# Kernel optimization log

Measured on AMD Instinct MI355X. Metric: run time of the kernel, lower is better.

The kernel has to match this reference:

```python
import jax, jax.numpy as jnp
import numpy as np

N, M, D_IN, H1, D, OUT_C = 2048, 128, 352, 512, 256, 13


def _lin_bn_relu(x, w, b, g, be):
    # 1x1 conv == linear over last dim; BN (eval) folded to per-channel affine (g, be)
    return jax.nn.relu(g * (x @ w.T + b) + be)


def _encode(x, wA, bA, gA, beA, wB, bB, gB, beB):
    return _lin_bn_relu(_lin_bn_relu(x, wA, bA, gA, beA), wB, bB, gB, beB)


def setup_inputs() -> dict:
    key = jax.random.key(0)
    ks = iter(jax.random.split(key, 64))

    def wgt(shape, s=0.05):
        return (jax.random.normal(next(ks), shape, jnp.float32) * s)

    def gamma(c):
        return 1.0 + 0.05 * jax.random.normal(next(ks), (c,), jnp.float32)

    inp = {}
    inp['ext_fea'] = jax.random.normal(next(ks), (N, D_IN), jnp.float32)
    inp['lab_fea'] = jax.random.normal(next(ks), (M, D_IN), jnp.float32)
    # convs1: 352->512->256, each Conv1d(1x1)+BN+ReLU
    inp.update(w1a=wgt((H1, D_IN)), b1a=wgt((H1,)), g1a=gamma(H1), be1a=wgt((H1,)))
    inp.update(w1b=wgt((D, H1)), b1b=wgt((D,)), g1b=gamma(D), be1b=wgt((D,)))
    # convs2: same shapes
    inp.update(w2a=wgt((H1, D_IN)), b2a=wgt((H1,)), g2a=gamma(H1), be2a=wgt((H1,)))
    inp.update(w2b=wgt((D, H1)), b2b=wgt((D,)), g2b=gamma(D), be2b=wgt((D,)))
    # wei_conv SharedMLP [256,32,64,256]: three Conv2d(1x1)+BN+ReLU
    inp.update(mw1=wgt((32, D)), mb1=wgt((32,)), mg1=gamma(32), mbe1=wgt((32,)))
    inp.update(mw2=wgt((64, 32)), mb2=wgt((64,)), mg2=gamma(64), mbe2=wgt((64,)))
    inp.update(mw3=wgt((D, 64)), mb3=wgt((D,)), mg3=gamma(D), mbe3=wgt((D,)))
    # fc
    inp.update(fcw=wgt((OUT_C, D)), fcb=wgt((OUT_C,)))
    return inp


def reference(ext_fea, lab_fea,
              w1a, b1a, g1a, be1a, w1b, b1b, g1b, be1b,
              w2a, b2a, g2a, be2a, w2b, b2b, g2b, be2b,
              mw1, mb1, mg1, mbe1, mw2, mb2, mg2, mbe2, mw3, mb3, mg3, mbe3,
              fcw, fcb):
    A = _encode(ext_fea, w1a, b1a, g1a, be1a, w1b, b1b, g1b, be1b)   # [N, 256]
    B = _encode(lab_fea, w2a, b2a, g2a, be2a, w2b, b2b, g2b, be2b)   # [M, 256]
    diff = A[:, None, :] - B[None, :, :]                             # [N, M, 256]
    h = _lin_bn_relu(diff, mw1, mb1, mg1, mbe1)                      # [N, M, 32]
    h = _lin_bn_relu(h, mw2, mb2, mg2, mbe2)                         # [N, M, 64]
    wei = _lin_bn_relu(h, mw3, mb3, mg3, mbe3)                       # [N, M, 256]
    # torch softmax over dim=-1 of [1,256,N,M] == over M == axis 1 here
    wei = jax.nn.softmax(wei, axis=1)
    att = jnp.sum(wei * diff, axis=1)                                # [N, 256]
    return att @ fcw.T + fcb                                         # [N, 13]
```

## Files before the change

### kernel.cpp

```cpp
#include <hip/hip_runtime.h>
#include <stdint.h>


typedef __attribute__((ext_vector_type(4))) float float4_t;
typedef __attribute__((ext_vector_type(4))) float f32x4;
typedef __attribute__((ext_vector_type(8))) short bf16x8;
typedef __attribute__((ext_vector_type(8))) unsigned short ushort8_t;
typedef unsigned short ushort_t;

__device__ __forceinline__ unsigned short f2b(float f) {
  union { float f; unsigned int i; } v; v.f = f;
  unsigned int x = v.i;
  return (unsigned short)((x + 0x7FFFu + ((x >> 16) & 1u)) >> 16);
}

template<int ISBF>
__device__ __forceinline__ ushort8_t ld8(const void* base, size_t idx) {
  if constexpr (ISBF) {
    return *(const ushort8_t*)((const ushort_t*)base + idx);
  } else {
    const float* p = (const float*)base + idx;
    float4_t v0 = *(const float4_t*)p;
    float4_t v1 = *(const float4_t*)(p + 4);
    ushort8_t u;
    #pragma unroll
    for (int e = 0; e < 4; ++e) { u[e] = f2b(v0[e]); u[4 + e] = f2b(v1[e]); }
    return u;
  }
}

template<int XBF, int WBF, int OUT_BF16>
__global__ __launch_bounds__(256) void enc_mfma(
    const void* __restrict__ XA, const void* __restrict__ WA,
    const float* __restrict__ bA, const float* __restrict__ gA, const float* __restrict__ beA,
    void* __restrict__ YA,
    const void* __restrict__ XB, const void* __restrict__ WB,
    const float* __restrict__ bB, const float* __restrict__ gB, const float* __restrict__ beB,
    void* __restrict__ YB, float* __restrict__ YBT,
    int J, int K, int nbxA)
{
  __shared__ ushort_t Xs[2][32][40];
  __shared__ ushort_t Ws[2][32][40];
  const int bx = blockIdx.x, by = blockIdx.y;
  const void* X; const void* W;
  const float *bb, *gg, *bev; void* Y; int i0, isB;
  if (bx < nbxA) { X = XA; W = WA; bb = bA; gg = gA; bev = beA; Y = YA; i0 = bx * 32; isB = 0; }
  else           { X = XB; W = WB; bb = bB; gg = gB; bev = beB; Y = YB; i0 = (bx - nbxA) * 32; isB = 1; }
  const int j0 = by * 32;
  const int tid = threadIdx.x, w = tid >> 6, lane = tid & 63, lg = lane >> 4, lr = lane & 15;
  const int mt = w >> 1, ct = w & 1;
  const int row = tid >> 2, k8 = (tid & 3) * 8;

  f32x4 acc = f32x4{0.f, 0.f, 0.f, 0.f};

  ushort8_t sv = (row < 32) ? ld8<XBF>(X, (size_t)(i0 + row) * K + k8)
                            : ld8<WBF>(W, (size_t)(j0 + row - 32) * K + k8);
  for (int kt = 0; kt < K; kt += 32) {
    const int buf = (kt >> 5) & 1;
    if (row < 32) *(ushort8_t*)&Xs[buf][row][k8] = sv;
    else          *(ushort8_t*)&Ws[buf][row - 32][k8] = sv;
    __syncthreads();
    if (kt + 32 < K)
      sv = (row < 32) ? ld8<XBF>(X, (size_t)(i0 + row) * K + kt + 32 + k8)
                      : ld8<WBF>(W, (size_t)(j0 + row - 32) * K + kt + 32 + k8);
    bf16x8 af = *(const bf16x8*)&Xs[buf][mt * 16 + lr][lg * 8];
    bf16x8 bf_ = *(const bf16x8*)&Ws[buf][ct * 16 + lr][lg * 8];
    acc = __builtin_amdgcn_mfma_f32_16x16x32_bf16(af, bf_, acc, 0, 0, 0);
  }
  const int c = j0 + ct * 16 + lr;
  const float g = gg[c], bv = bb[c], ev = bev[c];
  #pragma unroll
  for (int r = 0; r < 4; ++r) {
    const int rowo = i0 + mt * 16 + 4 * lg + r;
    float t = fmaxf(g * (acc[r] + bv) + ev, 0.f);
    if (OUT_BF16) ((ushort_t*)Y)[(size_t)rowo * J + c] = f2b(t);
    else {
      ((float*)Y)[(size_t)rowo * J + c] = t;
      if (isB && YBT) YBT[(size_t)c * 128 + rowo] = t;
    }
  }
}

__global__ __launch_bounds__(256) void proj32(
    const float* __restrict__ Aenc, const float* __restrict__ Benc,
    const float* __restrict__ mw1, const float* __restrict__ mb1,
    const float* __restrict__ mg1, const float* __restrict__ mbe1,
    float* __restrict__ PA2, float* __restrict__ PB2, int nbxA,
    const float* __restrict__ mw2, const float* __restrict__ mw3,
    ushort_t* __restrict__ mw2b, ushort_t* __restrict__ mw3b)
{
  __shared__ float ps[4][32];
  const int tid = threadIdx.x, bx = blockIdx.x;
  if (bx >= nbxA + 32) {
    const int g = (bx - nbxA - 32) * 256 + tid;
    const float* s; ushort_t* d; int j;
    if (g < 256) { s = mw2; d = mw2b; j = g; }
    else         { s = mw3; d = mw3b; j = g - 256; }
    float4_t v0 = *(const float4_t*)&s[(size_t)j * 8];
    float4_t v1 = *(const float4_t*)&s[(size_t)j * 8 + 4];
    ushort8_t u;
    #pragma unroll
    for (int e = 0; e < 4; ++e) { u[e] = f2b(v0[e]); u[4 + e] = f2b(v1[e]); }
    *(ushort8_t*)&d[(size_t)j * 8] = u;
    return;
  }
  const float* X; float* P; int n0, wb;
  if (bx < nbxA) { X = Aenc; P = PA2; n0 = bx * 4; wb = 1; }
  else           { X = Benc; P = PB2; n0 = (bx - nbxA) * 4; wb = 0; }
  const int k = tid & 31, r = (tid >> 5) & 3, half = tid >> 7;
  const int n = n0 + r;
  const float* xp = &X[(size_t)n * 256 + half * 128];
  const float* wp = &mw1[k * 256 + half * 128];
  float s = 0.f;
  #pragma unroll 8
  for (int q = 0; q < 128; q += 4) {
    float4_t xv = *(const float4_t*)&xp[q];
    float4_t wv = *(const float4_t*)&wp[q];
    #pragma unroll
    for (int e = 0; e < 4; ++e) s = fmaf(xv[e], wv[e], s);
  }
  if (half == 1) ps[r][k] = s;
  __syncthreads();
  if (half == 0) {
    s += ps[r][k];
    P[(size_t)n * 32 + k] = wb ? (mg1[k] * (s + mb1[k]) + mbe1[k]) : (mg1[k] * s);
  }
}

__global__ __launch_bounds__(256, 2) void main_attn(
    const float* __restrict__ PA2, const float* __restrict__ PB2,
    const float* __restrict__ A, const float* __restrict__ BmT,
    const ushort_t* __restrict__ mw2b, const float* __restrict__ mb2,
    const float* __restrict__ mg2, const float* __restrict__ mbe2,
    const ushort_t* __restrict__ mw3b, const float* __restrict__ mb3,
    const float* __restrict__ mg3, const float* __restrict__ mbe3,
    const float* __restrict__ fcw, const float* __restrict__ fcb,
    float* __restrict__ outp)
{
  __shared__ __align__(16) char smem[40576];
  float* attLs = (float*)(smem + 36864);
  float* part  = (float*)(smem + 38912);

  const int tid = threadIdx.x;
  const int w = tid >> 6, lane = tid & 63, lg = lane >> 4, lr = lane & 15;
  const int n0 = blockIdx.x * 2;
  const float LOG2E = 1.4426950408889634f;

  float g2h[4], b2h[4], e2h[4];
  #pragma unroll
  for (int jt = 0; jt < 4; ++jt) {
    const int j = jt * 16 + lr;
    g2h[jt] = mg2[j]; b2h[jt] = mb2[j]; e2h[jt] = mbe2[j];
  }
  float gs3[4], cs3[4];
  #pragma unroll
  for (int ct = 0; ct < 4; ++ct) {
    const int c = w * 64 + ct * 16 + lr;
    const float g = mg3[c];
    gs3[ct] = g * LOG2E;
    cs3[ct] = (g * mb3[c] + mbe3[c]) * LOG2E;
  }

  #pragma unroll
  for (int nn = 0; nn < 2; ++nn) {
    const int n = n0 + nn;
    ushort_t* h2s = (ushort_t*)(smem + nn * 18432);

    {
      f32x4 acc1[2][4];
      #pragma unroll
      for (int mt = 0; mt < 2; ++mt)
        #pragma unroll
        for (int jt = 0; jt < 4; ++jt) acc1[mt][jt] = f32x4{0.f, 0.f, 0.f, 0.f};
      bf16x8 a1[2], b1[4];
      {
        const float* pa = &PA2[(size_t)n * 32 + lg * 8];
        float4_t pa0 = *(const float4_t*)pa;
        float4_t pa1 = *(const float4_t*)(pa + 4);
        #pragma unroll
        for (int mt = 0; mt < 2; ++mt) {
          const int m = w * 32 + mt * 16 + lr;
          const float* pb = &PB2[(size_t)m * 32 + lg * 8];
          float4_t pb0 = *(const float4_t*)pb;
          float4_t pb1 = *(const float4_t*)(pb + 4);
          bf16x8 u;
          #pragma unroll
          for (int e = 0; e < 4; ++e) {
            u[e]     = (short)f2b(fmaxf(pa0[e] - pb0[e], 0.f));
            u[4 + e] = (short)f2b(fmaxf(pa1[e] - pb1[e], 0.f));
          }
          a1[mt] = u;
        }
      }
      #pragma unroll
      for (int jt = 0; jt < 4; ++jt)
        b1[jt] = *(const bf16x8*)&mw2b[(jt * 16 + lr) * 32 + lg * 8];
      #pragma unroll
      for (int mt = 0; mt < 2; ++mt)
        #pragma unroll
        for (int jt = 0; jt < 4; ++jt)
          acc1[mt][jt] = __builtin_amdgcn_mfma_f32_16x16x32_bf16(a1[mt], b1[jt], acc1[mt][jt], 0, 0, 0);
      #pragma unroll
      for (int jt = 0; jt < 4; ++jt) {
        #pragma unroll
        for (int mt = 0; mt < 2; ++mt)
          #pragma unroll
          for (int r = 0; r < 4; ++r)
            h2s[(w * 32 + mt * 16 + 4 * lg + r) * 72 + jt * 16 + lr] =
                f2b(fmaxf(g2h[jt] * (acc1[mt][jt][r] + b2h[jt]) + e2h[jt], 0.f));
      }
    }
    __syncthreads();

    float smv[4], wbv[4];
    #pragma unroll
    for (int cp = 0; cp < 2; ++cp) {
      f32x4 acc[8][2];
      #pragma unroll
      for (int mt = 0; mt < 8; ++mt) {
        acc[mt][0] = f32x4{0.f, 0.f, 0.f, 0.f};
        acc[mt][1] = f32x4{0.f, 0.f, 0.f, 0.f};
      }
      #pragma unroll
      for (int ks = 0; ks < 2; ++ks) {
        bf16x8 bfr[2];
        #pragma unroll
        for (int q = 0; q < 2; ++q) {
          const int c = w * 64 + (cp * 2 + q) * 16 + lr;
          bfr[q] = *(const bf16x8*)&mw3b[(size_t)c * 64 + ks * 32 + lg * 8];
        }
        #pragma unroll
        for (int mt = 0; mt < 8; ++mt) {
          bf16x8 af = *(const bf16x8*)&h2s[(mt * 16 + lr) * 72 + ks * 32 + lg * 8];
          acc[mt][0] = __builtin_amdgcn_mfma_f32_16x16x32_bf16(af, bfr[0], acc[mt][0], 0, 0, 0);
          acc[mt][1] = __builtin_amdgcn_mfma_f32_16x16x32_bf16(af, bfr[1], acc[mt][1], 0, 0, 0);
        }
      }
      #pragma unroll
      for (int q = 0; q < 2; ++q) {
        const int ct = cp * 2 + q;
        const int c = w * 64 + ct * 16 + lr;
        f32x4 sm4 = f32x4{0.f, 0.f, 0.f, 0.f};
        f32x4 wb4 = f32x4{0.f, 0.f, 0.f, 0.f};
        #pragma unroll
        for (int mt = 0; mt < 8; ++mt) {
          float4_t bv4 = *(const float4_t*)&BmT[(size_t)c * 128 + mt * 16 + 4 * lg];
          #pragma unroll
          for (int r = 0; r < 4; ++r) {
            float t = fmaf(gs3[ct], acc[mt][q][r], cs3[ct]);
            float p = exp2f(__builtin_amdgcn_fmed3f(t, 0.f, 80.f));
            sm4[r] += p;
            wb4[r] = fmaf(p, bv4[r], wb4[r]);
          }
        }
        smv[ct] = (sm4[0] + sm4[1]) + (sm4[2] + sm4[3]);
        wbv[ct] = (wb4[0] + wb4[1]) + (wb4[2] + wb4[3]);
      }
    }
    #pragma unroll
    for (int st = 16; st <= 32; st <<= 1) {
      #pragma unroll
      for (int ct = 0; ct < 4; ++ct) {
        smv[ct] += __shfl_xor(smv[ct], st, 64);
        wbv[ct] += __shfl_xor(wbv[ct], st, 64);
      }
    }
    if (lg == 0) {
      #pragma unroll
      for (int ct = 0; ct < 4; ++ct) {
        const int c = w * 64 + ct * 16 + lr;
        attLs[nn * 256 + c] = A[(size_t)n * 256 + c] - wbv[ct] / smv[ct];
      }
    }
  }
  __syncthreads();

  {
    const int o = tid >> 4, gp = tid & 15;
    if (o < 13) {
      float4_t wv[4];
      #pragma unroll
      for (int i = 0; i < 4; ++i)
        wv[i] = *(const float4_t*)&fcw[(size_t)o * 256 + gp * 16 + i * 4];
      #pragma unroll
      for (int nn = 0; nn < 2; ++nn) {
        float s = 0.f;
        #pragma unroll
        for (int i = 0; i < 4; ++i) {
          float4_t av = *(const float4_t*)&attLs[nn * 256 + gp * 16 + i * 4];
          #pragma unroll
          for (int e = 0; e < 4; ++e) s = fmaf(av[e], wv[i][e], s);
        }
        part[nn * 208 + o * 16 + gp] = s;
      }
    }
  }
  __syncthreads();
  if (tid < 26) {
    const int nn = tid / 13, o = tid % 13;
    float s = fcb[o];
    #pragma unroll
    for (int gp = 0; gp < 16; ++gp) s += part[nn * 208 + o * 16 + gp];
    outp[(size_t)(n0 + nn) * 13 + o] = s;
  }
}

extern "C" void kernel_launch(void* const* d_in, const int* in_sizes, int n_in,
                              void* d_out, int out_size, void* d_ws, size_t ws_size,
                              hipStream_t stream)
{
  const float* ext = (const float*)d_in[0];
  const float* lab = (const float*)d_in[1];
  const float* w1a = (const float*)d_in[2];
  const float* b1a = (const float*)d_in[3];
  const float* g1a = (const float*)d_in[4];
  const float* be1a= (const float*)d_in[5];
  const float* w1b = (const float*)d_in[6];
  const float* b1b = (const float*)d_in[7];
  const float* g1b = (const float*)d_in[8];
  const float* be1b= (const float*)d_in[9];
  const float* w2a = (const float*)d_in[10];
  const float* b2a = (const float*)d_in[11];
  const float* g2a = (const float*)d_in[12];
  const float* be2a= (const float*)d_in[13];
  const float* w2b = (const float*)d_in[14];
  const float* b2b = (const float*)d_in[15];
  const float* g2b = (const float*)d_in[16];
  const float* be2b= (const float*)d_in[17];
  const float* mw1 = (const float*)d_in[18];
  const float* mb1 = (const float*)d_in[19];
  const float* mg1 = (const float*)d_in[20];
  const float* mbe1= (const float*)d_in[21];
  const float* mw2 = (const float*)d_in[22];
  const float* mb2 = (const float*)d_in[23];
  const float* mg2 = (const float*)d_in[24];
  const float* mbe2= (const float*)d_in[25];
  const float* mw3 = (const float*)d_in[26];
  const float* mb3 = (const float*)d_in[27];
  const float* mg3 = (const float*)d_in[28];
  const float* mbe3= (const float*)d_in[29];
  const float* fcw = (const float*)d_in[30];
  const float* fcb = (const float*)d_in[31];

  char* ws = (char*)d_ws;
  ushort_t* Y1ab = (ushort_t*)(ws);
  float*    PA2  = (float*)(ws);
  float*    PB2  = (float*)(ws + 262144);
  float*    Aenc = (float*)(ws + (2u << 20));
  char* b5 = ws + (4u << 20);
  ushort_t* mw2b = (ushort_t*)(b5);
  ushort_t* mw3b = (ushort_t*)(b5 + 4096);
  ushort_t* Y1bb = (ushort_t*)(b5 + 36864);
  float*    Benc = (float*)(b5 + 167936);
  float*    BencT= (float*)(b5 + 299008);

  enc_mfma<0, 0, 1><<<dim3(68, 16), 256, 0, stream>>>(
      (const void*)ext, (const void*)w1a, b1a, g1a, be1a, (void*)Y1ab,
      (const void*)lab, (const void*)w2a, b2a, g2a, be2a, (void*)Y1bb,
      (float*)nullptr, 512, 352, 64);
  enc_mfma<1, 0, 0><<<dim3(68, 8), 256, 0, stream>>>(
      (const void*)Y1ab, (const void*)w1b, b1b, g1b, be1b, (void*)Aenc,
      (const void*)Y1bb, (const void*)w2b, b2b, g2b, be2b, (void*)Benc,
      BencT, 256, 512, 64);
  proj32<<<553, 256, 0, stream>>>(Aenc, Benc, mw1, mb1, mg1, mbe1, PA2, PB2, 512,
                                  mw2, mw3, mw2b, mw3b);
  main_attn<<<1024, 256, 0, stream>>>(PA2, PB2, Aenc, BencT,
                                      mw2b, mb2, mg2, mbe2, mw3b, mb3, mg3, mbe3,
                                      fcw, fcb, (float*)d_out);
}
```

Baseline: 87.79 us.

## Double main attention block to 512 threads, halving per-wave channel work

The main attention kernel now runs 8 waves per block instead of 4. Each wave handles 16 rows of the first MFMA stage and 32 output channels of the second, instead of 32 and 64, so the two-pass channel loop goes away and per-thread accumulators shrink. The final FC reduction is spread over 32 partial sums per output. exp2f is also replaced by the raw hardware exp2 intrinsic. The aim is more parallelism and latency hiding per CU, at the cost of more threads sharing the same LDS tile and barriers.

Result: slower. 95.07 us (+8.3%).

```diff
diff --git a/kernel.cpp b/kernel.cpp
--- a/kernel.cpp
+++ b/kernel.cpp
@@ -127,7 +127,7 @@
   }
 }
 
-__global__ __launch_bounds__(256, 2) void main_attn(
+__global__ __launch_bounds__(512, 2) void main_attn(
     const float* __restrict__ PA2, const float* __restrict__ PB2,
     const float* __restrict__ A, const float* __restrict__ BmT,
     const ushort_t* __restrict__ mw2b, const float* __restrict__ mb2,
@@ -137,7 +137,7 @@
     const float* __restrict__ fcw, const float* __restrict__ fcb,
     float* __restrict__ outp)
 {
-  __shared__ __align__(16) char smem[40576];
+  __shared__ __align__(16) char smem[42240];
   float* attLs = (float*)(smem + 36864);
   float* part  = (float*)(smem + 38912);
 
@@ -152,10 +152,10 @@
     const int j = jt * 16 + lr;
     g2h[jt] = mg2[j]; b2h[jt] = mb2[j]; e2h[jt] = mbe2[j];
   }
-  float gs3[4], cs3[4];
+  float gs3[2], cs3[2];
   #pragma unroll
-  for (int ct = 0; ct < 4; ++ct) {
-    const int c = w * 64 + ct * 16 + lr;
+  for (int ct = 0; ct < 2; ++ct) {
+    const int c = w * 32 + ct * 16 + lr;
     const float g = mg3[c];
     gs3[ct] = g * LOG2E;
     cs3[ct] = (g * mb3[c] + mbe3[c]) * LOG2E;
@@ -167,131 +167,118 @@
     ushort_t* h2s = (ushort_t*)(smem + nn * 18432);
 
     {
-      f32x4 acc1[2][4];
-      #pragma unroll
-      for (int mt = 0; mt < 2; ++mt)
-        #pragma unroll
-        for (int jt = 0; jt < 4; ++jt) acc1[mt][jt] = f32x4{0.f, 0.f, 0.f, 0.f};
-      bf16x8 a1[2], b1[4];
+      f32x4 acc1[4];
+      #pragma unroll
+      for (int jt = 0; jt < 4; ++jt) acc1[jt] = f32x4{0.f, 0.f, 0.f, 0.f};
+      bf16x8 a1, b1[4];
       {
         const float* pa = &PA2[(size_t)n * 32 + lg * 8];
         float4_t pa0 = *(const float4_t*)pa;
         float4_t pa1 = *(const float4_t*)(pa + 4);
+        const int m = w * 16 + lr;
+        const float* pb = &PB2[(size_t)m * 32 + lg * 8];
+        float4_t pb0 = *(const float4_t*)pb;
+        float4_t pb1 = *(const float4_t*)(pb + 4);
+        bf16x8 u;
         #pragma unroll
-        for (int mt = 0; mt < 2; ++mt) {
-          const int m = w * 32 + mt * 16 + lr;
-          const float* pb = &PB2[(size_t)m * 32 + lg * 8];
-          float4_t pb0 = *(const float4_t*)pb;
-          float4_t pb1 = *(const float4_t*)(pb + 4);
-          bf16x8 u;
-          #pragma unroll
-          for (int e = 0; e < 4; ++e) {
-            u[e]     = (short)f2b(fmaxf(pa0[e] - pb0[e], 0.f));
-            u[4 + e] = (short)f2b(fmaxf(pa1[e] - pb1[e], 0.f));
-          }
-          a1[mt] = u;
+        for (int e = 0; e < 4; ++e) {
+          u[e]     = (short)f2b(fmaxf(pa0[e] - pb0[e], 0.f));
+          u[4 + e] = (short)f2b(fmaxf(pa1[e] - pb1[e], 0.f));
         }
+        a1 = u;
       }
       #pragma unroll
       for (int jt = 0; jt < 4; ++jt)
         b1[jt] = *(const bf16x8*)&mw2b[(jt * 16 + lr) * 32 + lg * 8];
       #pragma unroll
-      for (int mt = 0; mt < 2; ++mt)
+      for (int jt = 0; jt < 4; ++jt)
+        acc1[jt] = __builtin_amdgcn_mfma_f32_16x16x32_bf16(a1, b1[jt], acc1[jt], 0, 0, 0);
+      #pragma unroll
+      for (int jt = 0; jt < 4; ++jt)
         #pragma unroll
-        for (int jt = 0; jt < 4; ++jt)
-          acc1[mt][jt] = __builtin_amdgcn_mfma_f32_16x16x32_bf16(a1[mt], b1[jt], acc1[mt][jt], 0, 0, 0);
-      #pragma unroll
-      for (int jt = 0; jt < 4; ++jt) {
+        for (int r = 0; r < 4; ++r)
+          h2s[(w * 16 + 4 * lg + r) * 72 + jt * 16 + lr] =
+              f2b(fmaxf(g2h[jt] * (acc1[jt][r] + b2h[jt]) + e2h[jt], 0.f));
+    }
+    __syncthreads();
+
+    f32x4 acc[8][2];
+    #pragma unroll
+    for (int mt = 0; mt < 8; ++mt) {
+      acc[mt][0] = f32x4{0.f, 0.f, 0.f, 0.f};
+      acc[mt][1] = f32x4{0.f, 0.f, 0.f, 0.f};
+    }
+    #pragma unroll
+    for (int ks = 0; ks < 2; ++ks) {
+      bf16x8 bfr[2];
+      #pragma unroll
+      for (int q = 0; q < 2; ++q) {
+        const int c = w * 32 + q * 16 + lr;
+        bfr[q] = *(const bf16x8*)&mw3b[(size_t)c * 64 + ks * 32 + lg * 8];
+      }
+      #pragma unroll
+      for (int mt = 0; mt < 8; ++mt) {
+        bf16x8 af = *(const bf16x8*)&h2s[(mt * 16 + lr) * 72 + ks * 32 + lg * 8];
+        acc[mt][0] = __builtin_amdgcn_mfma_f32_16x16x32_bf16(af, bfr[0], acc[mt][0], 0, 0, 0);
+        acc[mt][1] = __builtin_amdgcn_mfma_f32_16x16x32_bf16(af, bfr[1], acc[mt][1], 0, 0, 0);
+      }
+    }
+
+    float smv[2], wbv[2];
+    #pragma unroll
+    for (int q = 0; q < 2; ++q) {
+      const int c = w * 32 + q * 16 + lr;
+      f32x4 sm4 = f32x4{0.f, 0.f, 0.f, 0.f};
+      f32x4 wb4 = f32x4{0.f, 0.f, 0.f, 0.f};
+      #pragma unroll
+      for (int mt = 0; mt < 8; ++mt) {
+        float4_t bv4 = *(const float4_t*)&BmT[(size_t)c * 128 + mt * 16 + 4 * lg];
         #pragma unroll
-        for (int mt = 0; mt < 2; ++mt)
-          #pragma unroll
-          for (int r = 0; r < 4; ++r)
-            h2s[(w * 32 + mt * 16 + 4 * lg + r) * 72 + jt * 16 + lr] =
-                f2b(fmaxf(g2h[jt] * (acc1[mt][jt][r] + b2h[jt]) + e2h[jt], 0.f));
-      }
-    }
-    __syncthreads();
-
-    float smv[4], wbv[4];
-    #pragma unroll
-    for (int cp = 0; cp < 2; ++cp) {
-      f32x4 acc[8][2];
-      #pragma unroll
-      for (int mt = 0; mt < 8; ++mt) {
-        acc[mt][0] = f32x4{0.f, 0.f, 0.f, 0.f};
-        acc[mt][1] = f32x4{0.f, 0.f, 0.f, 0.f};
-      }
-      #pragma unroll
-      for (int ks = 0; ks < 2; ++ks) {
-        bf16x8 bfr[2];
-        #pragma unroll
-        for (int q = 0; q < 2; ++q) {
-          const int c = w * 64 + (cp * 2 + q) * 16 + lr;
-          bfr[q] = *(const bf16x8*)&mw3b[(size_t)c * 64 + ks * 32 + lg * 8];
+        for (int r = 0; r < 4; ++r) {
+          float t = fmaf(gs3[q], acc[mt][q][r], cs3[q]);
+          float p = __builtin_amdgcn_exp2f(__builtin_amdgcn_fmed3f(t, 0.f, 80.f));
+          sm4[r] += p;
+          wb4[r] = fmaf(p, bv4[r], wb4[r]);
         }
-        #pragma unroll
-        for (int mt = 0; mt < 8; ++mt) {
-          bf16x8 af = *(const bf16x8*)&h2s[(mt * 16 + lr) * 72 + ks * 32 + lg * 8];
-          acc[mt][0] = __builtin_amdgcn_mfma_f32_16x16x32_bf16(af, bfr[0], acc[mt][0], 0, 0, 0);
-          acc[mt][1] = __builtin_amdgcn_mfma_f32_16x16x32_bf16(af, bfr[1], acc[mt][1], 0, 0, 0);
-        }
-      }
+      }
+      smv[q] = (sm4[0] + sm4[1]) + (sm4[2] + sm4[3]);
+      wbv[q] = (wb4[0] + wb4[1]) + (wb4[2] + wb4[3]);
+    }
+    #pragma unroll
+    for (int st = 16; st <= 32; st <<= 1) {
       #pragma unroll
       for (int q = 0; q < 2; ++q) {
-        const int ct = cp * 2 + q;
-        const int c = w * 64 + ct * 16 + lr;
-        f32x4 sm4 = f32x4{0.f, 0.f, 0.f, 0.f};
-        f32x4 wb4 = f32x4{0.f, 0.f, 0.f, 0.f};
-        #pragma unroll
-        for (int mt = 0; mt < 8; ++mt) {
-          float4_t bv4 = *(const float4_t*)&BmT[(size_t)c * 128 + mt * 16 + 4 * lg];
-          #pragma unroll
-          for (int r = 0; r < 4; ++r) {
-            float t = fmaf(gs3[ct], acc[mt][q][r], cs3[ct]);
-            float p = exp2f(__builtin_amdgcn_fmed3f(t, 0.f, 80.f));
-            sm4[r] += p;
-            wb4[r] = fmaf(p, bv4[r], wb4[r]);
-          }
-        }
-        smv[ct] = (sm4[0] + sm4[1]) + (sm4[2] + sm4[3]);
-        wbv[ct] = (wb4[0] + wb4[1]) + (wb4[2] + wb4[3]);
-      }
-    }
-    #pragma unroll
-    for (int st = 16; st <= 32; st <<= 1) {
-      #pragma unroll
-      for (int ct = 0; ct < 4; ++ct) {
-        smv[ct] += __shfl_xor(smv[ct], st, 64);
-        wbv[ct] += __shfl_xor(wbv[ct], st, 64);
+        smv[q] += __shfl_xor(smv[q], st, 64);
+        wbv[q] += __shfl_xor(wbv[q], st, 64);
       }
     }
     if (lg == 0) {
       #pragma unroll
-      for (int ct = 0; ct < 4; ++ct) {
-        const int c = w * 64 + ct * 16 + lr;
-        attLs[nn * 256 + c] = A[(size_t)n * 256 + c] - wbv[ct] / smv[ct];
+      for (int q = 0; q < 2; ++q) {
+        const int c = w * 32 + q * 16 + lr;
+        attLs[nn * 256 + c] = A[(size_t)n * 256 + c] - wbv[q] / smv[q];
       }
     }
   }
   __syncthreads();
 
   {
-    const int o = tid >> 4, gp = tid & 15;
+    const int o = tid >> 5, gp = tid & 31;
     if (o < 13) {
-      float4_t wv[4];
-      #pragma unroll
-      for (int i = 0; i < 4; ++i)
-        wv[i] = *(const float4_t*)&fcw[(size_t)o * 256 + gp * 16 + i * 4];
+      float4_t wv[2];
+      #pragma unroll
+      for (int i = 0; i < 2; ++i)
+        wv[i] = *(const float4_t*)&fcw[(size_t)o * 256 + gp * 8 + i * 4];
       #pragma unroll
       for (int nn = 0; nn < 2; ++nn) {
         float s = 0.f;
         #pragma unroll
-        for (int i = 0; i < 4; ++i) {
-          float4_t av = *(const float4_t*)&attLs[nn * 256 + gp * 16 + i * 4];
+        for (int i = 0; i < 2; ++i) {
+          float4_t av = *(const float4_t*)&attLs[nn * 256 + gp * 8 + i * 4];
           #pragma unroll
           for (int e = 0; e < 4; ++e) s = fmaf(av[e], wv[i][e], s);
         }
-        part[nn * 208 + o * 16 + gp] = s;
+        part[nn * 416 + o * 32 + gp] = s;
       }
     }
   }
@@ -300,7 +287,7 @@
     const int nn = tid / 13, o = tid % 13;
     float s = fcb[o];
     #pragma unroll
-    for (int gp = 0; gp < 16; ++gp) s += part[nn * 208 + o * 16 + gp];
+    for (int gp = 0; gp < 32; ++gp) s += part[nn * 416 + o * 32 + gp];
     outp[(size_t)(n0 + nn) * 13 + o] = s;
   }
 }
@@ -364,7 +351,7 @@
       BencT, 256, 512, 64);
   proj32<<<553, 256, 0, stream>>>(Aenc, Benc, mw1, mb1, mg1, mbe1, PA2, PB2, 512,
                                   mw2, mw3, mw2b, mw3b);
-  main_attn<<<1024, 256, 0, stream>>>(PA2, PB2, Aenc, BencT,
+  main_attn<<<1024, 512, 0, stream>>>(PA2, PB2, Aenc, BencT,
                                       mw2b, mb2, mg2, mbe2, mw3b, mb3, mg3, mbe3,
                                       fcw, fcb, (float*)d_out);
 }
```
